# Kernel optimization log

Hardware: AMD Instinct MI355X
Metric: run time of the kernel (lower is better)

The kernel has to match this reference:

```python
import jax, jax.numpy as jnp
import numpy as np

NBINS = 256       # kornia equalize_clahe default histogram bins
GRID = (8, 8)     # kornia default grid_size


def _clahe(x, clip_limit):
    """kornia-style CLAHE on x:(C,H,W) in [0,1]; H,W divisible by GRID."""
    C, H, W = x.shape
    GH, GW = GRID
    TH, TW = H // GH, W // GW
    pixels = TH * TW
    # ---- per-tile histograms via flat scatter-add (irregular core) ----
    b_hist = jnp.clip((x * NBINS).astype(jnp.int32), 0, NBINS - 1)  # torch.histc(min=0,max=1) bins
    tiles = b_hist.reshape(C, GH, TH, GW, TW).transpose(0, 1, 3, 2, 4).reshape(-1, pixels)
    ntiles = tiles.shape[0]  # C*GH*GW
    flat = (tiles + (jnp.arange(ntiles, dtype=jnp.int32) * NBINS)[:, None]).ravel()
    hist = jnp.zeros((ntiles * NBINS,), x.dtype).at[flat].add(1.0).reshape(ntiles, NBINS)
    # ---- clip and redistribute excess (kornia _compute_luts) ----
    max_val = jnp.maximum(jnp.floor(clip_limit * pixels / NBINS), 1.0)
    clipped = jnp.minimum(hist, max_val)
    excess = pixels - clipped.sum(-1)                    # (ntiles,), >= 0
    residual = jnp.mod(excess, NBINS)
    redist = (excess - residual) / NBINS
    hist = clipped + redist[:, None] + (jnp.arange(NBINS) < residual[:, None]).astype(x.dtype)
    # ---- LUT from CDF ----
    lut = jnp.floor(jnp.clip(jnp.cumsum(hist, -1) * (NBINS - 1) / pixels, 0, NBINS - 1))
    lut = lut.reshape(C, GH, GW, NBINS)
    # ---- per-pixel bilinear interpolation between 4 neighbouring tile LUTs ----
    def coords(n, T, G):
        g = (jnp.arange(n) + 0.5) / T - 0.5    # fractional tile coordinate
        lo = jnp.clip(jnp.floor(g), 0, G - 1).astype(jnp.int32)
        hi = jnp.clip(lo + 1, 0, G - 1)
        w = jnp.clip(g - jnp.floor(g), 0.0, 1.0).astype(x.dtype)
        return lo, hi, w
    y0, y1, wy = coords(H, TH, GH)
    x0, x1, wx = coords(W, TW, GW)
    b = jnp.clip(jnp.floor(x * (NBINS - 1)).astype(jnp.int32), 0, NBINS - 1)  # lookup bin
    c = jnp.arange(C)[:, None, None]
    def g(ty, tx):  # gather lut[c, ty[h], tx[w], b[c,h,w]] -> (C,H,W)
        return lut[c, ty[None, :, None], tx[None, None, :], b]
    top = g(y0, x0) * (1 - wx)[None, None, :] + g(y0, x1) * wx[None, None, :]
    bot = g(y1, x0) * (1 - wx)[None, None, :] + g(y1, x1) * wx[None, None, :]
    out = top * (1 - wy)[None, :, None] + bot * wy[None, :, None]
    return out / (NBINS - 1)


def _forward(x, log_cor=True):
    shape = x.shape
    mean = x.mean()
    std = jnp.std(x, ddof=1)            # torch .std() is unbiased
    x = (x - mean) / std                # TF.normalize
    xmin, xmax = x.min(), x.max()
    x = (x - xmin) / (xmax - xmin)      # normalize_in_range(x, 0, 1)
    ct_proxy = jnp.std(x, ddof=1)       # x.std([0,1,2]) on 3D input = scalar
    def clahe_branch(xx):
        beta = 10.0 * ct_proxy
        cl = 1.0 / (1.0 - beta) + beta  # data-dependent clip limit
        return _clahe(xx, cl)
    x = jax.lax.cond(ct_proxy < 0.05, clahe_branch, lambda xx: xx, x)
    if log_cor:
        x = jnp.log2(1.0 + x)           # adjust_log with gain=1
    return x.reshape(shape)


def setup_inputs() -> dict:
    key = jax.random.key(0)
    x = jax.random.normal(key, (32, 1024, 1024), dtype=jnp.float32)
    # heavy-tailed distribution -> std/range (ct_proxy) ~ 0.01 < 0.05 so CLAHE branch runs
    x = x ** 3
    return {"x": x}


def reference(x):
    return _forward(x, log_cor=True)
```

## Files before the change

### kernel.cpp

```cpp
#include <hip/hip_runtime.h>
#include <math.h>

#define NC 32
#define NH 1024
#define NW 1024
#define NTH 128
#define NTW 128
#define NBINS 256
#define NTILES (NC*8*8)
#define NPIXTOT (NC*NH*NW)
#define TPIX (NTH*NTW)

#define OFF_PSUM   0
#define OFF_PSQ    16384
#define OFF_PMIN   32768
#define OFF_PMAX   40960
#define OFF_PARAMS 49152
#define OFF_LUT8   65536

__global__ __launch_bounds__(256) void k_reduce(const float* __restrict__ x,
                                                double* __restrict__ ps,
                                                double* __restrict__ ps2,
                                                float* __restrict__ pmn,
                                                float* __restrict__ pmx) {
    int tid = threadIdx.x;
    long g = (long)blockIdx.x * 256 + tid;
    double sA = 0.0, sB = 0.0, sC = 0.0, sD = 0.0;
    double qA = 0.0, qB = 0.0, qC = 0.0, qD = 0.0;
    float mn = INFINITY, mx = -INFINITY;
    const float4* x4 = (const float4*)x;
    const long S = (long)2048 * 256;
    for (long i = g; i < (long)(NPIXTOT / 4); i += 4 * S) {
        float4 a = x4[i];
        float4 b = x4[i + S];
        float4 c = x4[i + 2 * S];
        float4 d = x4[i + 3 * S];
        sA += (double)((a.x + a.y) + (a.z + a.w));
        qA += (double)fmaf(a.x, a.x, fmaf(a.y, a.y, fmaf(a.z, a.z, a.w * a.w)));
        sB += (double)((b.x + b.y) + (b.z + b.w));
        qB += (double)fmaf(b.x, b.x, fmaf(b.y, b.y, fmaf(b.z, b.z, b.w * b.w)));
        sC += (double)((c.x + c.y) + (c.z + c.w));
        qC += (double)fmaf(c.x, c.x, fmaf(c.y, c.y, fmaf(c.z, c.z, c.w * c.w)));
        sD += (double)((d.x + d.y) + (d.z + d.w));
        qD += (double)fmaf(d.x, d.x, fmaf(d.y, d.y, fmaf(d.z, d.z, d.w * d.w)));
        mn = fminf(mn, fminf(fminf(fminf(a.x, a.y), fminf(a.z, a.w)),
                             fminf(fminf(b.x, b.y), fminf(b.z, b.w))));
        mn = fminf(mn, fminf(fminf(fminf(c.x, c.y), fminf(c.z, c.w)),
                             fminf(fminf(d.x, d.y), fminf(d.z, d.w))));
        mx = fmaxf(mx, fmaxf(fmaxf(fmaxf(a.x, a.y), fmaxf(a.z, a.w)),
                             fmaxf(fmaxf(b.x, b.y), fmaxf(b.z, b.w))));
        mx = fmaxf(mx, fmaxf(fmaxf(fmaxf(c.x, c.y), fmaxf(c.z, c.w)),
                             fmaxf(fmaxf(d.x, d.y), fmaxf(d.z, d.w))));
    }
    double s = (sA + sB) + (sC + sD);
    double s2 = (qA + qB) + (qC + qD);
    for (int o = 32; o; o >>= 1) {
        s  += __shfl_down(s, o);
        s2 += __shfl_down(s2, o);
        mn = fminf(mn, __shfl_down(mn, o));
        mx = fmaxf(mx, __shfl_down(mx, o));
    }
    __shared__ double shs[4], shs2[4];
    __shared__ float shmn[4], shmx[4];
    int wid = tid >> 6, lane = tid & 63;
    if (lane == 0) { shs[wid] = s; shs2[wid] = s2; shmn[wid] = mn; shmx[wid] = mx; }
    __syncthreads();
    if (tid == 0) {
        ps[blockIdx.x]  = shs[0] + shs[1] + shs[2] + shs[3];
        ps2[blockIdx.x] = shs2[0] + shs2[1] + shs2[2] + shs2[3];
        pmn[blockIdx.x] = fminf(fminf(shmn[0], shmn[1]), fminf(shmn[2], shmn[3]));
        pmx[blockIdx.x] = fmaxf(fmaxf(shmx[0], shmx[1]), fmaxf(shmx[2], shmx[3]));
    }
}

__global__ __launch_bounds__(256) void k_histlut(const float* __restrict__ x,
                                                 const double* __restrict__ ps,
                                                 const double* __restrict__ ps2,
                                                 const float* __restrict__ pmn,
                                                 const float* __restrict__ pmx,
                                                 float* __restrict__ params,
                                                 unsigned char* __restrict__ lut8) {
    __shared__ unsigned lh[4 * NBINS];
    __shared__ int sh[NBINS];
    __shared__ double shs[4], shs2[4];
    __shared__ float shmn[4], shmx[4], spar[4];
    int tid = threadIdx.x;
    int t = blockIdx.x;
    int lane = tid & 63;
    int wid = tid >> 6;

    double s = 0.0, s2 = 0.0;
    float mn = INFINITY, mx = -INFINITY;
    for (int i = tid; i < 2048; i += 256) {
        s += ps[i]; s2 += ps2[i];
        mn = fminf(mn, pmn[i]); mx = fmaxf(mx, pmx[i]);
    }
    for (int o = 32; o; o >>= 1) {
        s  += __shfl_down(s, o);
        s2 += __shfl_down(s2, o);
        mn = fminf(mn, __shfl_down(mn, o));
        mx = fmaxf(mx, __shfl_down(mx, o));
    }
    if (lane == 0) { shs[wid] = s; shs2[wid] = s2; shmn[wid] = mn; shmx[wid] = mx; }
    __syncthreads();
    if (tid == 0) {
        double S  = shs[0] + shs[1] + shs[2] + shs[3];
        double S2 = shs2[0] + shs2[1] + shs2[2] + shs2[3];
        float MN = fminf(fminf(shmn[0], shmn[1]), fminf(shmn[2], shmn[3]));
        float MX = fmaxf(fmaxf(shmx[0], shmx[1]), fmaxf(shmx[2], shmx[3]));
        const double n = (double)NPIXTOT;
        double var = (S2 - S * S / n) / (n - 1.0);
        double sd = sqrt(var > 0.0 ? var : 0.0);
        double range = (double)MX - (double)MN;
        double ct = sd / range;
        int flag = (ct < 0.05) ? 1 : 0;
        double beta = 10.0 * ct;
        double cl = 1.0 / (1.0 - beta) + beta;
        double mv = floor(cl * (double)TPIX / (double)NBINS);
        if (mv < 1.0) mv = 1.0;
        spar[0] = MN;
        spar[1] = (float)(1.0 / range);
        spar[2] = (float)mv;
        if (t == 0) {
            params[0] = MN;
            params[1] = (float)(1.0 / range);
            params[2] = (float)mv;
            ((int*)params)[3] = flag;
        }
    }
    #pragma unroll
    for (int w = 0; w < 4; w++) lh[w * NBINS + tid] = 0;
    __syncthreads();
    float xmin = spar[0], inv = spar[1];
    int mv = (int)spar[2];

    int c = t >> 6, gy = (t >> 3) & 7, gx = t & 7;
    const float* base = x + ((long)c * NH + (long)gy * NTH) * NW + gx * NTW;
    unsigned* mylh = lh + wid * NBINS;
    #pragma unroll 4
    for (int j = 0; j < 16; j++) {
        int l = j * 256 + tid;
        int th = l >> 5, tw4 = l & 31;
        float4 v = *(const float4*)(base + (long)th * NW + tw4 * 4);
        int b0 = (int)((v.x - xmin) * inv * 256.0f); b0 = b0 < 0 ? 0 : (b0 > 255 ? 255 : b0);
        int b1 = (int)((v.y - xmin) * inv * 256.0f); b1 = b1 < 0 ? 0 : (b1 > 255 ? 255 : b1);
        int b2 = (int)((v.z - xmin) * inv * 256.0f); b2 = b2 < 0 ? 0 : (b2 > 255 ? 255 : b2);
        int b3 = (int)((v.w - xmin) * inv * 256.0f); b3 = b3 < 0 ? 0 : (b3 > 255 ? 255 : b3);
        int d = __builtin_amdgcn_readfirstlane(b0);
        int cnt = (b0 == d) + (b1 == d) + (b2 == d) + (b3 == d);
        #pragma unroll
        for (int m = 1; m < 64; m <<= 1) cnt += __shfl_xor(cnt, m);
        if (lane == 0 && cnt > 0) atomicAdd(&mylh[d], (unsigned)cnt);
        if (b0 != d) atomicAdd(&mylh[b0], 1u);
        if (b1 != d) atomicAdd(&mylh[b1], 1u);
        if (b2 != d) atomicAdd(&mylh[b2], 1u);
        if (b3 != d) atomicAdd(&mylh[b3], 1u);
    }
    __syncthreads();

    int h = (int)(lh[tid] + lh[NBINS + tid] + lh[2 * NBINS + tid] + lh[3 * NBINS + tid]);
    int cl = h < mv ? h : mv;
    sh[tid] = cl;
    __syncthreads();
    for (int o = 1; o < NBINS; o <<= 1) {
        int v = (tid >= o) ? sh[tid - o] : 0;
        __syncthreads();
        sh[tid] += v;
        __syncthreads();
    }
    int total = sh[NBINS - 1];
    int cdfc = sh[tid];
    int excess = TPIX - total;
    int residual = excess & (NBINS - 1);
    int redist = excess >> 8;
    int cdf = cdfc + redist * (tid + 1) + ((tid + 1) < residual ? (tid + 1) : residual);
    float lv = floorf(fminf((float)cdf * 255.0f / 16384.0f, 255.0f));
    int iv = (int)(lv < 0.0f ? 0.0f : lv);
    lut8[t * NBINS + tid] = (unsigned char)iv;
}

__global__ __launch_bounds__(256) void k_out(const float* __restrict__ x,
                                             const float* __restrict__ params,
                                             const unsigned char* __restrict__ lut8,
                                             float* __restrict__ out) {
    __shared__ unsigned char slut[4096];
    int tid = threadIdx.x;
    int g = blockIdx.x;
    int c = g >> 8;
    int h0 = (g & 255) << 2;
    float xmin = params[0], inv = params[1];
    int flag = ((const int*)params)[3];
    float gy0 = (h0 + 0.5f) * (1.0f / NTH) - 0.5f;
    float fy0 = floorf(gy0);
    int y0 = (int)fy0; y0 = y0 < 0 ? 0 : (y0 > 7 ? 7 : y0);
    int y1 = y0 + 1 > 7 ? 7 : y0 + 1;
    const unsigned char* src0 = lut8 + ((long)c * 64 + y0 * 8) * NBINS;
    const unsigned char* src1 = lut8 + ((long)c * 64 + y1 * 8) * NBINS;
    if (tid < 128) {
        *(uint4*)(slut + tid * 16) = *(const uint4*)(src0 + tid * 16);
    } else {
        int u = tid - 128;
        *(uint4*)(slut + 2048 + u * 16) = *(const uint4*)(src1 + u * 16);
    }
    const float* base = x + ((long)c << 20) + ((long)h0 << 10) + tid * 4;
    float4 v0 = *(const float4*)(base);
    float4 v1 = *(const float4*)(base + 1024);
    float4 v2 = *(const float4*)(base + 2048);
    float4 v3 = *(const float4*)(base + 3072);
    int xo0[4], xo1[4]; float wx[4];
    #pragma unroll
    for (int k = 0; k < 4; k++) {
        int wk = tid * 4 + k;
        float gxc = (wk + 0.5f) * (1.0f / NTW) - 0.5f;
        float fx = floorf(gxc);
        wx[k] = gxc - fx;
        int xx = (int)fx; xx = xx < 0 ? 0 : (xx > 7 ? 7 : xx);
        xo0[k] = xx * NBINS;
        xo1[k] = (xx + 1 > 7 ? 7 : xx + 1) * NBINS;
    }
    __syncthreads();
    float4 vv[4] = {v0, v1, v2, v3};
    #pragma unroll
    for (int r = 0; r < 4; r++) {
        int h = h0 + r;
        float gyf = (h + 0.5f) * (1.0f / NTH) - 0.5f;
        float wy = gyf - floorf(gyf);
        float4 v = vv[r];
        float zf[4] = {v.x, v.y, v.z, v.w};
        float o4[4];
        #pragma unroll
        for (int k = 0; k < 4; k++) {
            float z = (zf[k] - xmin) * inv;
            float val;
            if (flag) {
                int b = (int)(z * 255.0f);
                b = b < 0 ? 0 : (b > 255 ? 255 : b);
                float l00 = (float)slut[xo0[k] + b];
                float l01 = (float)slut[xo1[k] + b];
                float l10 = (float)slut[2048 + xo0[k] + b];
                float l11 = (float)slut[2048 + xo1[k] + b];
                float top = l00 * (1.0f - wx[k]) + l01 * wx[k];
                float bot = l10 * (1.0f - wx[k]) + l11 * wx[k];
                val = (top * (1.0f - wy) + bot * wy) * (1.0f / 255.0f);
            } else {
                val = z;
            }
            o4[k] = __log2f(1.0f + val);
        }
        *(float4*)(out + ((long)c << 20) + ((long)h << 10) + tid * 4) =
            make_float4(o4[0], o4[1], o4[2], o4[3]);
    }
}

extern "C" void kernel_launch(void* const* d_in, const int* in_sizes, int n_in,
                              void* d_out, int out_size, void* d_ws, size_t ws_size,
                              hipStream_t stream) {
    const float* x = (const float*)d_in[0];
    float* out = (float*)d_out;
    char* ws = (char*)d_ws;
    double* ps   = (double*)(ws + OFF_PSUM);
    double* ps2  = (double*)(ws + OFF_PSQ);
    float* pmn   = (float*)(ws + OFF_PMIN);
    float* pmx   = (float*)(ws + OFF_PMAX);
    float* params= (float*)(ws + OFF_PARAMS);
    unsigned char* lut8 = (unsigned char*)(ws + OFF_LUT8);

    k_reduce<<<2048, 256, 0, stream>>>(x, ps, ps2, pmn, pmx);
    k_histlut<<<NTILES, 256, 0, stream>>>(x, ps, ps2, pmn, pmx, params, lut8);
    k_out<<<NC * 256, 256, 0, stream>>>(x, params, lut8, out);
}
```

Before: 306.9 us.

## Cache 8-bit lookup bin indices in histogram pass and reuse in output pass

The histogram kernel now computes each pixel's lookup bin index and writes it as a byte array to workspace. The output kernel then reads these bytes instead of re-reading the float input, cutting its input traffic from 4 bytes to 1 byte per pixel when CLAHE runs. The histogram's shared-memory atomics also switch to ballot-based wave aggregation of up to three distinct bins per step. This adds a 32 MB byte write and extra ballot and shuffle work to the histogram kernel, and the byte array must fit in the workspace.

```diff
diff --git a/kernel.cpp b/kernel.cpp
--- a/kernel.cpp
+++ b/kernel.cpp
@@ -17,6 +17,7 @@
 #define OFF_PMAX   40960
 #define OFF_PARAMS 49152
 #define OFF_LUT8   65536
+#define OFF_IDX8   1048576
 
 __global__ __launch_bounds__(256) void k_reduce(const float* __restrict__ x,
                                                 double* __restrict__ ps,
@@ -79,7 +80,8 @@
                                                  const float* __restrict__ pmn,
                                                  const float* __restrict__ pmx,
                                                  float* __restrict__ params,
-                                                 unsigned char* __restrict__ lut8) {
+                                                 unsigned char* __restrict__ lut8,
+                                                 unsigned char* __restrict__ idx8) {
     __shared__ unsigned lh[4 * NBINS];
     __shared__ int sh[NBINS];
     __shared__ double shs[4], shs2[4];
@@ -135,26 +137,46 @@
     int mv = (int)spar[2];
 
     int c = t >> 6, gy = (t >> 3) & 7, gx = t & 7;
-    const float* base = x + ((long)c * NH + (long)gy * NTH) * NW + gx * NTW;
+    long tilebase = ((long)c * NH + (long)gy * NTH) * NW + gx * NTW;
+    const float* base = x + tilebase;
+    unsigned char* ibase = idx8 + tilebase;
     unsigned* mylh = lh + wid * NBINS;
-    #pragma unroll 4
+    #pragma unroll 2
     for (int j = 0; j < 16; j++) {
         int l = j * 256 + tid;
         int th = l >> 5, tw4 = l & 31;
-        float4 v = *(const float4*)(base + (long)th * NW + tw4 * 4);
-        int b0 = (int)((v.x - xmin) * inv * 256.0f); b0 = b0 < 0 ? 0 : (b0 > 255 ? 255 : b0);
-        int b1 = (int)((v.y - xmin) * inv * 256.0f); b1 = b1 < 0 ? 0 : (b1 > 255 ? 255 : b1);
-        int b2 = (int)((v.z - xmin) * inv * 256.0f); b2 = b2 < 0 ? 0 : (b2 > 255 ? 255 : b2);
-        int b3 = (int)((v.w - xmin) * inv * 256.0f); b3 = b3 < 0 ? 0 : (b3 > 255 ? 255 : b3);
-        int d = __builtin_amdgcn_readfirstlane(b0);
-        int cnt = (b0 == d) + (b1 == d) + (b2 == d) + (b3 == d);
+        long rowoff = (long)th * NW + tw4 * 4;
+        float4 v = *(const float4*)(base + rowoff);
+        float z0 = (v.x - xmin) * inv;
+        float z1 = (v.y - xmin) * inv;
+        float z2 = (v.z - xmin) * inv;
+        float z3 = (v.w - xmin) * inv;
+        int b0 = (int)(z0 * 256.0f); b0 = b0 < 0 ? 0 : (b0 > 255 ? 255 : b0);
+        int b1 = (int)(z1 * 256.0f); b1 = b1 < 0 ? 0 : (b1 > 255 ? 255 : b1);
+        int b2 = (int)(z2 * 256.0f); b2 = b2 < 0 ? 0 : (b2 > 255 ? 255 : b2);
+        int b3 = (int)(z3 * 256.0f); b3 = b3 < 0 ? 0 : (b3 > 255 ? 255 : b3);
+        int i0 = (int)(z0 * 255.0f); i0 = i0 < 0 ? 0 : (i0 > 255 ? 255 : i0);
+        int i1 = (int)(z1 * 255.0f); i1 = i1 < 0 ? 0 : (i1 > 255 ? 255 : i1);
+        int i2 = (int)(z2 * 255.0f); i2 = i2 < 0 ? 0 : (i2 > 255 ? 255 : i2);
+        int i3 = (int)(z3 * 255.0f); i3 = i3 < 0 ? 0 : (i3 > 255 ? 255 : i3);
+        *(uchar4*)(ibase + rowoff) = make_uchar4((unsigned char)i0, (unsigned char)i1,
+                                                 (unsigned char)i2, (unsigned char)i3);
+        int bs[4] = {b0, b1, b2, b3};
         #pragma unroll
-        for (int m = 1; m < 64; m <<= 1) cnt += __shfl_xor(cnt, m);
-        if (lane == 0 && cnt > 0) atomicAdd(&mylh[d], (unsigned)cnt);
-        if (b0 != d) atomicAdd(&mylh[b0], 1u);
-        if (b1 != d) atomicAdd(&mylh[b1], 1u);
-        if (b2 != d) atomicAdd(&mylh[b2], 1u);
-        if (b3 != d) atomicAdd(&mylh[b3], 1u);
+        for (int k = 0; k < 4; k++) {
+            int b = bs[k];
+            unsigned long long alive = __ballot(1);
+            #pragma unroll
+            for (int r = 0; r < 3; r++) {
+                if (!alive) break;
+                int leader = (int)(__ffsll((long long)alive) - 1);
+                int lb = __shfl(b, leader);
+                unsigned long long m = __ballot(b == lb) & alive;
+                if (lane == leader) atomicAdd(&mylh[lb], (unsigned)__popcll(m));
+                alive &= ~m;
+            }
+            if ((alive >> lane) & 1ull) atomicAdd(&mylh[b], 1u);
+        }
     }
     __syncthreads();
 
@@ -182,6 +204,7 @@
 __global__ __launch_bounds__(256) void k_out(const float* __restrict__ x,
                                              const float* __restrict__ params,
                                              const unsigned char* __restrict__ lut8,
+                                             const unsigned char* __restrict__ idx8,
                                              float* __restrict__ out) {
     __shared__ unsigned char slut[4096];
     int tid = threadIdx.x;
@@ -202,50 +225,63 @@
         int u = tid - 128;
         *(uint4*)(slut + 2048 + u * 16) = *(const uint4*)(src1 + u * 16);
     }
-    const float* base = x + ((long)c << 20) + ((long)h0 << 10) + tid * 4;
-    float4 v0 = *(const float4*)(base);
-    float4 v1 = *(const float4*)(base + 1024);
-    float4 v2 = *(const float4*)(base + 2048);
-    float4 v3 = *(const float4*)(base + 3072);
-    int xo0[4], xo1[4]; float wx[4];
+    long pbase = ((long)c << 20) + ((long)h0 << 10) + tid * 4;
+    uchar4 iv0, iv1, iv2, iv3;
+    float4 v0, v1, v2, v3;
+    if (flag) {
+        const uchar4* ib = (const uchar4*)(idx8 + pbase);
+        iv0 = ib[0]; iv1 = ib[256]; iv2 = ib[512]; iv3 = ib[768];
+    } else {
+        const float* base = x + pbase;
+        v0 = *(const float4*)(base);
+        v1 = *(const float4*)(base + 1024);
+        v2 = *(const float4*)(base + 2048);
+        v3 = *(const float4*)(base + 3072);
+    }
+    int xo0[4], xo1[4]; float wx[4], owx[4];
     #pragma unroll
     for (int k = 0; k < 4; k++) {
         int wk = tid * 4 + k;
         float gxc = (wk + 0.5f) * (1.0f / NTW) - 0.5f;
         float fx = floorf(gxc);
         wx[k] = gxc - fx;
+        owx[k] = 1.0f - wx[k];
         int xx = (int)fx; xx = xx < 0 ? 0 : (xx > 7 ? 7 : xx);
         xo0[k] = xx * NBINS;
         xo1[k] = (xx + 1 > 7 ? 7 : xx + 1) * NBINS;
     }
     __syncthreads();
+    uchar4 ivv[4] = {iv0, iv1, iv2, iv3};
     float4 vv[4] = {v0, v1, v2, v3};
     #pragma unroll
     for (int r = 0; r < 4; r++) {
         int h = h0 + r;
         float gyf = (h + 0.5f) * (1.0f / NTH) - 0.5f;
         float wy = gyf - floorf(gyf);
-        float4 v = vv[r];
-        float zf[4] = {v.x, v.y, v.z, v.w};
         float o4[4];
-        #pragma unroll
-        for (int k = 0; k < 4; k++) {
-            float z = (zf[k] - xmin) * inv;
-            float val;
-            if (flag) {
-                int b = (int)(z * 255.0f);
-                b = b < 0 ? 0 : (b > 255 ? 255 : b);
+        if (flag) {
+            uchar4 ivr = ivv[r];
+            int bb[4] = {ivr.x, ivr.y, ivr.z, ivr.w};
+            #pragma unroll
+            for (int k = 0; k < 4; k++) {
+                int b = bb[k];
                 float l00 = (float)slut[xo0[k] + b];
                 float l01 = (float)slut[xo1[k] + b];
                 float l10 = (float)slut[2048 + xo0[k] + b];
                 float l11 = (float)slut[2048 + xo1[k] + b];
-                float top = l00 * (1.0f - wx[k]) + l01 * wx[k];
-                float bot = l10 * (1.0f - wx[k]) + l11 * wx[k];
-                val = (top * (1.0f - wy) + bot * wy) * (1.0f / 255.0f);
-            } else {
-                val = z;
+                float top = l00 * owx[k] + l01 * wx[k];
+                float bot = l10 * owx[k] + l11 * wx[k];
+                float val = (top * (1.0f - wy) + bot * wy) * (1.0f / 255.0f);
+                o4[k] = __log2f(1.0f + val);
             }
-            o4[k] = __log2f(1.0f + val);
+        } else {
+            float4 v = vv[r];
+            float zf[4] = {v.x, v.y, v.z, v.w};
+            #pragma unroll
+            for (int k = 0; k < 4; k++) {
+                float z = (zf[k] - xmin) * inv;
+                o4[k] = __log2f(1.0f + z);
+            }
         }
         *(float4*)(out + ((long)c << 20) + ((long)h << 10) + tid * 4) =
             make_float4(o4[0], o4[1], o4[2], o4[3]);
@@ -264,8 +300,9 @@
     float* pmx   = (float*)(ws + OFF_PMAX);
     float* params= (float*)(ws + OFF_PARAMS);
     unsigned char* lut8 = (unsigned char*)(ws + OFF_LUT8);
+    unsigned char* idx8 = (unsigned char*)(ws + OFF_IDX8);
 
     k_reduce<<<2048, 256, 0, stream>>>(x, ps, ps2, pmn, pmx);
-    k_histlut<<<NTILES, 256, 0, stream>>>(x, ps, ps2, pmn, pmx, params, lut8);
-    k_out<<<NC * 256, 256, 0, stream>>>(x, params, lut8, out);
+    k_histlut<<<NTILES, 256, 0, stream>>>(x, ps, ps2, pmn, pmx, params, lut8, idx8);
+    k_out<<<NC * 256, 256, 0, stream>>>(x, params, lut8, idx8, out);
 }
```

After: 295.5 us. 1.04x faster.
